# Kernel optimization log

Hardware: AMD Instinct MI355X
Metric: run time of the kernel (lower is better)

## Reference

```python
import jax, jax.numpy as jnp
import numpy as np

HEADS = 4
RATES = (1, 2, 3, 4)
BN_EPS = 1e-5


def setup_inputs() -> dict:
    key = jax.random.key(0)
    k1, k2, k3 = jax.random.split(key, 3)
    b, c, h, w = 4, 256, 128, 128
    x = jax.random.normal(k1, (b, c, h, w), dtype=jnp.float32)
    w_qkv = jax.random.normal(k2, (3 * c, c), dtype=jnp.float32) * 0.02
    w_proj = jax.random.normal(k3, (c, c), dtype=jnp.float32) * 0.02
    gamma = jnp.ones((c,), dtype=jnp.float32)
    beta = jnp.zeros((c,), dtype=jnp.float32)
    return {"x": x, "w_qkv": w_qkv, "w_proj": w_proj, "gamma": gamma, "beta": beta}


def _neighbors(t, r, h, w):
    # t: [b, d, h, w] -> [b, d, 9, h, w], 3x3 dilated window with zero padding
    # (row-major kernel-position order matches F.unfold's C x kh x kw layout).
    tp = jnp.pad(t, ((0, 0), (0, 0), (r, r), (r, r)))
    return jnp.stack(
        [tp[:, :, i * r:i * r + h, j * r:j * r + w] for i in range(3) for j in range(3)],
        axis=2,
    )


def reference(x, w_qkv, w_proj, gamma, beta):
    b, c, h, w = x.shape
    d = c // HEADS
    # 1x1 conv == channel matmul
    qkv = jnp.einsum('oc,bchw->bohw', w_qkv, x)
    q, k, v = jnp.split(qkv, 3, axis=1)
    q = q.reshape(b, HEADS, d, h, w)
    k = k.reshape(b, HEADS, d, h, w)
    v = v.reshape(b, HEADS, d, h, w)
    outs = []
    for hi, r in enumerate(RATES):
        qh = q[:, hi]                      # [b, d, h, w]
        k_n = _neighbors(k[:, hi], r, h, w)  # [b, d, 9, h, w]
        v_n = _neighbors(v[:, hi], r, h, w)  # [b, d, 9, h, w]
        scores = jnp.einsum('bdhw,bdnhw->bnhw', qh, k_n)  # [b, 9, h, w]
        attn = jax.nn.softmax(scores, axis=1)
        outs.append(jnp.einsum('bdnhw,bnhw->bdhw', v_n, attn))
    y = jnp.concatenate(outs, axis=1)      # [b, c, h, w]
    y = jnp.einsum('oc,bchw->bohw', w_proj, y)
    # BatchNorm2d (training-mode batch statistics, biased variance)
    mean = y.mean(axis=(0, 2, 3), keepdims=True)
    var = ((y - mean) ** 2).mean(axis=(0, 2, 3), keepdims=True)
    yn = (y - mean) * jax.lax.rsqrt(var + BN_EPS)
    yn = yn * gamma[None, :, None, None] + beta[None, :, None, None]
    return x + jax.nn.silu(yn)
```

## Files before the change

kernel.cpp:

```cpp
#include <hip/hip_runtime.h>
#include <hip/hip_bf16.h>

#define BATCH 4
#define CCH   256
#define HH    128
#define WW    128
#define HWSZ  (HH * WW)
#define NHEADS 4
#define DHEAD 64
#define KDIM  256
#define PDIM  16384

typedef unsigned short u16;
typedef short bf16x8 __attribute__((ext_vector_type(8)));
typedef float f32x4  __attribute__((ext_vector_type(4)));

__device__ __forceinline__ float bf2f(u16 u) {
    return __uint_as_float(((unsigned)u) << 16);
}
__device__ __forceinline__ u16 f2bf(float f) {
    unsigned u = __float_as_uint(f);
    unsigned r = (u + 0x7fffu + ((u >> 16) & 1u)) >> 16;
    return (u16)r;
}
__device__ __forceinline__ unsigned pack2(float a, float b) {
    return (unsigned)f2bf(a) | ((unsigned)f2bf(b) << 16);
}
__device__ __forceinline__ void gl_lds16(const u16* g, u16* l) {
    __builtin_amdgcn_global_load_lds(
        (const __attribute__((address_space(1))) void*)g,
        (__attribute__((address_space(3))) void*)l, 16, 0, 0);
}

__global__ __launch_bounds__(256) void wconv(
    const float* __restrict__ wq, const float* __restrict__ wp,
    u16* __restrict__ wqb, u16* __restrict__ wpb)
{
    const int i = (blockIdx.x * 256 + threadIdx.x) * 4;
    const float4 v = (i < 196608)
        ? *reinterpret_cast<const float4*>(&wq[i])
        : *reinterpret_cast<const float4*>(&wp[i - 196608]);
    ushort4 o;
    o.x = f2bf(v.x); o.y = f2bf(v.y); o.z = f2bf(v.z); o.w = f2bf(v.w);
    if (i < 196608) *reinterpret_cast<ushort4*>(&wqb[i]) = o;
    else            *reinterpret_cast<ushort4*>(&wpb[i - 196608]) = o;
}

__global__ __launch_bounds__(256) void transpose_x(
    const float* __restrict__ x, u16* __restrict__ XT)
{
    __shared__ float t[32][33];
    const int b  = blockIdx.z;
    const int c0 = blockIdx.y * 32;
    const int p0 = blockIdx.x * 32;
    const int tid = threadIdx.x;

    #pragma unroll
    for (int it = 0; it < 4; ++it) {
        const int r = it * 8 + (tid >> 5);
        const int col = tid & 31;
        t[r][col] = x[((size_t)b * CCH + c0 + r) * HWSZ + p0 + col];
    }
    __syncthreads();
    #pragma unroll
    for (int it = 0; it < 2; ++it) {
        const int prow = it * 16 + (tid >> 4);
        const int cpair = (tid & 15) * 2;
        const float v0 = t[cpair][prow];
        const float v1 = t[cpair + 1][prow];
        ushort2 o; o.x = f2bf(v0); o.y = f2bf(v1);
        *reinterpret_cast<ushort2*>(
            &XT[((size_t)b * HWSZ + p0 + prow) * CCH + c0 + cpair]) = o;
    }
}

__global__ __launch_bounds__(256) void gemm_qkv(
    const u16* __restrict__ A, const u16* __restrict__ B,
    u16* __restrict__ QKVH, long long b_zs)
{
    constexpr int BK = 64;
    constexpr int CTP = 72;
    __shared__ __align__(16) u16 lds[18432];
    u16* As = lds;
    u16* Bs = lds + 8192;

    const int tid  = threadIdx.x;
    const int lane = tid & 63;
    const int w    = tid >> 6;
    const int wm   = w >> 1, wn = w & 1;
    const int o0   = blockIdx.y * 128;
    const int p0   = blockIdx.x * 128;
    const int z    = blockIdx.z;
    const u16* Bz  = B + (size_t)z * b_zs;

    const int srow  = lane >> 3;
    const int sslot = (lane & 7) ^ srow;

    auto stage = [&](int c0) {
        #pragma unroll
        for (int j = 0; j < 4; ++j) {
            const int q = w * 4 + j;
            const int r = q * 8 + srow;
            gl_lds16(A  + (size_t)(o0 + r) * KDIM + c0 + sslot * 8, As + q * 512);
            gl_lds16(Bz + (size_t)(p0 + r) * KDIM + c0 + sslot * 8, Bs + q * 512);
        }
    };

    f32x4 acc[4][4];
    #pragma unroll
    for (int m = 0; m < 4; ++m)
        #pragma unroll
        for (int n = 0; n < 4; ++n)
            acc[m][n] = (f32x4){0.f, 0.f, 0.f, 0.f};

    stage(0);
    #pragma unroll
    for (int kt = 0; kt < KDIM / BK; ++kt) {
        __syncthreads();
        #pragma unroll
        for (int h = 0; h < 2; ++h) {
            bf16x8 af[4], bfr[4];
            #pragma unroll
            for (int m = 0; m < 4; ++m) {
                const int r  = wm * 64 + m * 16 + (lane & 15);
                const int sl = ((h << 2) | (lane >> 4)) ^ (r & 7);
                af[m] = *reinterpret_cast<const bf16x8*>(As + r * BK + sl * 8);
            }
            #pragma unroll
            for (int n = 0; n < 4; ++n) {
                const int r  = wn * 64 + n * 16 + (lane & 15);
                const int sl = ((h << 2) | (lane >> 4)) ^ (r & 7);
                bfr[n] = *reinterpret_cast<const bf16x8*>(Bs + r * BK + sl * 8);
            }
            #pragma unroll
            for (int m = 0; m < 4; ++m)
                #pragma unroll
                for (int n = 0; n < 4; ++n)
                    acc[m][n] = __builtin_amdgcn_mfma_f32_16x16x32_bf16(
                        af[m], bfr[n], acc[m][n], 0, 0, 0);
        }
        if (kt + 1 < KDIM / BK) {
            __syncthreads();
            stage((kt + 1) * BK);
        }
    }

    __syncthreads();
    u16* Ct = lds;
    const int g = lane >> 4, ln15 = lane & 15;
    #pragma unroll
    for (int m = 0; m < 4; ++m) {
        const int och = m * 16 + g * 4;
        #pragma unroll
        for (int n = 0; n < 4; ++n) {
            const int px = wn * 64 + n * 16 + ln15;
            uint2 w2;
            w2.x = pack2(acc[m][n][0], acc[m][n][1]);
            w2.y = pack2(acc[m][n][2], acc[m][n][3]);
            *reinterpret_cast<uint2*>(&Ct[(wm * 128 + px) * CTP + och]) = w2;
        }
    }
    __syncthreads();

    const int c   = tid & 7;
    const int sl  = (tid >> 3) & 1;
    const int px0 = tid >> 4;
    const int abs_slice = blockIdx.y * 2 + sl;
    const int qkv  = abs_slice >> 2;
    const int head = abs_slice & 3;
    u16* dbase = QKVH + ((size_t)(z * NHEADS + head) * HWSZ) * 192 + qkv * 64 + c * 8;
    #pragma unroll
    for (int pass = 0; pass < 8; ++pass) {
        const int px = px0 + pass * 16;
        const uint4 val = *reinterpret_cast<const uint4*>(
            &Ct[(sl * 128 + px) * CTP + c * 8]);
        *reinterpret_cast<uint4*>(dbase + (size_t)(p0 + px) * 192) = val;
    }
}

__global__ __launch_bounds__(256) void attn_proj(
    const u16* __restrict__ QKVH, const u16* __restrict__ WP,
    u16* __restrict__ YP, float* __restrict__ part, int batch0)
{
    __shared__ u16 y_lds[32][264];
    const int tid = threadIdx.x;
    const int z   = blockIdx.z;
    const int batch = batch0 + z;
    const int bxr = blockIdx.x;
    const int bx  = (bxr & 7) * 64 + (bxr >> 3);
    const int pxl = tid >> 3;
    const int oct = tid & 7;
    const int p   = bx * 32 + pxl;
    const int yy = p >> 7, xx = p & 127;

    #pragma unroll 1
    for (int hi = 0; hi < NHEADS; ++hi) {
        const int r = hi + 1;
        const u16* base = QKVH + ((size_t)(z * NHEADS + hi) * HWSZ) * 192;

        const uint4 qv = *reinterpret_cast<const uint4*>(
            base + (size_t)p * 192 + oct * 8);
        float qf[8];
        {
            const unsigned wv[4] = {qv.x, qv.y, qv.z, qv.w};
            #pragma unroll
            for (int d = 0; d < 4; ++d) {
                qf[d * 2 + 0] = __uint_as_float(wv[d] << 16);
                qf[d * 2 + 1] = __uint_as_float(wv[d] & 0xffff0000u);
            }
        }

        int offs[9]; float valid[9];
        #pragma unroll
        for (int n = 0; n < 9; ++n) {
            const int dy = (n / 3 - 1) * r;
            const int dx = (n % 3 - 1) * r;
            const int y2 = yy + dy, x2 = xx + dx;
            const bool ok = (y2 >= 0) && (y2 < HH) && (x2 >= 0) && (x2 < WW);
            valid[n] = ok ? 1.f : 0.f;
            const int y2c = min(max(y2, 0), HH - 1);
            const int x2c = min(max(x2, 0), WW - 1);
            offs[n] = y2c * WW + x2c;
        }

        float sc[9];
        #pragma unroll
        for (int n = 0; n < 9; ++n) {
            const uint4 kv = *reinterpret_cast<const uint4*>(
                base + (size_t)offs[n] * 192 + 64 + oct * 8);
            const unsigned wv[4] = {kv.x, kv.y, kv.z, kv.w};
            float s = 0.f;
            #pragma unroll
            for (int d = 0; d < 4; ++d) {
                s += qf[d * 2 + 0] * __uint_as_float(wv[d] << 16);
                s += qf[d * 2 + 1] * __uint_as_float(wv[d] & 0xffff0000u);
            }
            sc[n] = s;
        }
        #pragma unroll
        for (int n = 0; n < 9; ++n) {
            sc[n] += __shfl_xor(sc[n], 1);
            sc[n] += __shfl_xor(sc[n], 2);
            sc[n] += __shfl_xor(sc[n], 4);
            sc[n] *= valid[n];
        }

        float m = sc[0];
        #pragma unroll
        for (int n = 1; n < 9; ++n) m = fmaxf(m, sc[n]);
        float wgt[9], den = 0.f;
        #pragma unroll
        for (int n = 0; n < 9; ++n) { wgt[n] = __expf(sc[n] - m); den += wgt[n]; }
        const float inv = 1.f / den;
        #pragma unroll
        for (int n = 0; n < 9; ++n) wgt[n] *= inv * valid[n];

        float a[8];
        #pragma unroll
        for (int d = 0; d < 8; ++d) a[d] = 0.f;
        #pragma unroll
        for (int n = 0; n < 9; ++n) {
            const uint4 vv = *reinterpret_cast<const uint4*>(
                base + (size_t)offs[n] * 192 + 128 + oct * 8);
            const unsigned wv[4] = {vv.x, vv.y, vv.z, vv.w};
            const float wn_ = wgt[n];
            #pragma unroll
            for (int d = 0; d < 4; ++d) {
                a[d * 2 + 0] += wn_ * __uint_as_float(wv[d] << 16);
                a[d * 2 + 1] += wn_ * __uint_as_float(wv[d] & 0xffff0000u);
            }
        }
        uint4 st;
        st.x = pack2(a[0], a[1]);
        st.y = pack2(a[2], a[3]);
        st.z = pack2(a[4], a[5]);
        st.w = pack2(a[6], a[7]);
        *reinterpret_cast<uint4*>(&y_lds[pxl][hi * 64 + oct * 8]) = st;
    }
    __syncthreads();

    const int lane = tid & 63;
    const int w    = tid >> 6;
    const int ln15 = lane & 15, grp = lane >> 4;

    f32x4 acc[4][2];
    #pragma unroll
    for (int m = 0; m < 4; ++m)
        #pragma unroll
        for (int n = 0; n < 2; ++n)
            acc[m][n] = (f32x4){0.f, 0.f, 0.f, 0.f};

    #pragma unroll
    for (int ks = 0; ks < 8; ++ks) {
        bf16x8 bfr[2];
        #pragma unroll
        for (int n = 0; n < 2; ++n) {
            const int px = n * 16 + ln15;
            bfr[n] = *reinterpret_cast<const bf16x8*>(
                &y_lds[px][(ks * 4 + grp) * 8]);
        }
        bf16x8 af[4];
        #pragma unroll
        for (int m = 0; m < 4; ++m) {
            const int row = w * 64 + m * 16 + ln15;
            af[m] = *reinterpret_cast<const bf16x8*>(
                WP + (size_t)row * 256 + ks * 32 + grp * 8);
        }
        #pragma unroll
        for (int m = 0; m < 4; ++m)
            #pragma unroll
            for (int n = 0; n < 2; ++n)
                acc[m][n] = __builtin_amdgcn_mfma_f32_16x16x32_bf16(
                    af[m], bfr[n], acc[m][n], 0, 0, 0);
    }

    u16* Yz = YP + (size_t)batch * CCH * HWSZ;
    float sums[4][4], sqs[4][4];
    #pragma unroll
    for (int m = 0; m < 4; ++m) {
        const int row = w * 64 + m * 16 + grp * 4;
        #pragma unroll
        for (int j = 0; j < 4; ++j) {
            const float v0 = acc[m][0][j], v1 = acc[m][1][j];
            sums[m][j] = v0 + v1;
            sqs[m][j]  = v0 * v0 + v1 * v1;
        }
        #pragma unroll
        for (int n = 0; n < 2; ++n) {
            const int pc = bx * 32 + n * 16 + ln15;
            #pragma unroll
            for (int j = 0; j < 4; ++j)
                Yz[(size_t)(row + j) * PDIM + pc] = f2bf(acc[m][n][j]);
        }
    }
    #pragma unroll
    for (int mask = 1; mask <= 8; mask <<= 1)
        #pragma unroll
        for (int m = 0; m < 4; ++m)
            #pragma unroll
            for (int j = 0; j < 4; ++j) {
                sums[m][j] += __shfl_xor(sums[m][j], mask);
                sqs[m][j]  += __shfl_xor(sqs[m][j],  mask);
            }
    if (ln15 == 0) {
        const int blk = batch * 512 + bx;
        #pragma unroll
        for (int m = 0; m < 4; ++m) {
            const int row = w * 64 + m * 16 + grp * 4;
            #pragma unroll
            for (int j = 0; j < 4; ++j) {
                const size_t idx = ((size_t)(row + j) * 2048 + blk) * 2;
                part[idx]     = sums[m][j];
                part[idx + 1] = sqs[m][j];
            }
        }
    }
}

__global__ __launch_bounds__(256) void bn_final(
    const float* __restrict__ part, float* __restrict__ stats)
{
    const int c = blockIdx.x;
    const int tid = threadIdx.x;
    float s = 0.f, q = 0.f;
    #pragma unroll
    for (int it = 0; it < 8; ++it) {
        const int i = tid + it * 256;
        s += part[((size_t)c * 2048 + i) * 2 + 0];
        q += part[((size_t)c * 2048 + i) * 2 + 1];
    }
    __shared__ float sh0[256], sh1[256];
    sh0[tid] = s; sh1[tid] = q;
    __syncthreads();
    for (int st = 128; st > 0; st >>= 1) {
        if (tid < st) { sh0[tid] += sh0[tid + st]; sh1[tid] += sh1[tid + st]; }
        __syncthreads();
    }
    if (tid == 0) {
        const float N = (float)(BATCH * HWSZ);
        const float mean = sh0[0] / N;
        const float var  = sh1[0] / N - mean * mean;
        stats[c]       = mean;
        stats[CCH + c] = rsqrtf(var + 1e-5f);
    }
}

__global__ __launch_bounds__(256) void bn_silu_res(
    const u16* __restrict__ yp, const float* __restrict__ x,
    const float* __restrict__ stats, const float* __restrict__ gamma,
    const float* __restrict__ beta, float* __restrict__ out)
{
    const size_t i = ((size_t)blockIdx.x * 256 + threadIdx.x) * 8;
    const int c = (int)((i >> 14) & 255);
    const float mean = stats[c];
    const float inv  = stats[CCH + c];
    const float g = gamma[c], bt = beta[c];

    const uint4 yv = *reinterpret_cast<const uint4*>(&yp[i]);
    const unsigned wv[4] = {yv.x, yv.y, yv.z, yv.w};
    float vo[8];
    #pragma unroll
    for (int d = 0; d < 4; ++d) {
        const float y0 = __uint_as_float(wv[d] << 16);
        const float y1 = __uint_as_float(wv[d] & 0xffff0000u);
        const float yn0 = (y0 - mean) * inv * g + bt;
        const float yn1 = (y1 - mean) * inv * g + bt;
        vo[d * 2 + 0] = yn0 / (1.f + __expf(-yn0));
        vo[d * 2 + 1] = yn1 / (1.f + __expf(-yn1));
    }
    const float4 x0 = *reinterpret_cast<const float4*>(&x[i]);
    const float4 x1 = *reinterpret_cast<const float4*>(&x[i + 4]);
    float4 o0, o1;
    o0.x = x0.x + vo[0]; o0.y = x0.y + vo[1];
    o0.z = x0.z + vo[2]; o0.w = x0.w + vo[3];
    o1.x = x1.x + vo[4]; o1.y = x1.y + vo[5];
    o1.z = x1.z + vo[6]; o1.w = x1.w + vo[7];
    *reinterpret_cast<float4*>(&out[i])     = o0;
    *reinterpret_cast<float4*>(&out[i + 4]) = o1;
}

extern "C" void kernel_launch(void* const* d_in, const int* in_sizes, int n_in,
                              void* d_out, int out_size, void* d_ws, size_t ws_size,
                              hipStream_t stream)
{
    const float* x      = (const float*)d_in[0];
    const float* w_qkv  = (const float*)d_in[1];
    const float* w_proj = (const float*)d_in[2];
    const float* gamma  = (const float*)d_in[3];
    const float* beta   = (const float*)d_in[4];
    float* out = (float*)d_out;

    u16*   XT    = (u16*)d_ws;
    u16*   YP    = XT;
    u16*   WQb   = XT + (size_t)BATCH * HWSZ * CCH;
    u16*   WPb   = WQb + 768 * CCH;
    float* part  = (float*)(WPb + CCH * CCH);
    float* stats = part + (size_t)CCH * 2048 * 2;
    u16*   QKVH2 = (u16*)(stats + 512);

    wconv<<<256, 256, 0, stream>>>(w_qkv, w_proj, WQb, WPb);

    transpose_x<<<dim3(HWSZ / 32, CCH / 32, BATCH), 256, 0, stream>>>(x, XT);

    for (int pair = 0; pair < 2; ++pair) {
        const u16* Bx = XT + (size_t)pair * 2 * HWSZ * CCH;
        gemm_qkv<<<dim3(PDIM / 128, 768 / 128, 2), 256, 0, stream>>>(
            WQb, Bx, QKVH2, (long long)HWSZ * CCH);

        attn_proj<<<dim3(HWSZ / 32, 1, 2), 256, 0, stream>>>(
            QKVH2, WPb, YP, part, pair * 2);
    }

    bn_final<<<CCH, 256, 0, stream>>>(part, stats);

    bn_silu_res<<<(unsigned)((size_t)BATCH * CCH * HWSZ / 8 / 256), 256, 0, stream>>>(
        YP, x, stats, gamma, beta, out);
}
```

Before: 163.3 us.

## Assign one head per wave and two lanes per pixel in attention stage

The neighborhood-attention stage of attn_proj no longer loops serially over the four heads with eight lanes per pixel. Each wave now handles one head, and each pixel's 64-dim head is split across two lanes of 32 channels. This removes the head loop and two of the three shuffle-reduction steps, and gives each thread larger contiguous loads. In exchange it raises register use (32-float q and accumulator arrays) and changes the memory access pattern, which could lower occupancy.

```diff
diff --git a/kernel.cpp b/kernel.cpp
--- a/kernel.cpp
+++ b/kernel.cpp
@@ -188,25 +188,29 @@
     const int batch = batch0 + z;
     const int bxr = blockIdx.x;
     const int bx  = (bxr & 7) * 64 + (bxr >> 3);
-    const int pxl = tid >> 3;
-    const int oct = tid & 7;
-    const int p   = bx * 32 + pxl;
-    const int yy = p >> 7, xx = p & 127;
-
-    #pragma unroll 1
-    for (int hi = 0; hi < NHEADS; ++hi) {
-        const int r = hi + 1;
+    const int lane = tid & 63;
+    const int w    = tid >> 6;
+
+    {
+        const int hi   = w;
+        const int pxl  = lane >> 1;
+        const int half = lane & 1;
+        const int p    = bx * 32 + pxl;
+        const int yy = p >> 7, xx = p & 127;
+        const int r  = hi + 1;
         const u16* base = QKVH + ((size_t)(z * NHEADS + hi) * HWSZ) * 192;
 
-        const uint4 qv = *reinterpret_cast<const uint4*>(
-            base + (size_t)p * 192 + oct * 8);
-        float qf[8];
-        {
-            const unsigned wv[4] = {qv.x, qv.y, qv.z, qv.w};
+        const uint4* qp = reinterpret_cast<const uint4*>(
+            base + (size_t)p * 192 + half * 32);
+        float qf[32];
+        #pragma unroll
+        for (int c4 = 0; c4 < 4; ++c4) {
+            const uint4 t = qp[c4];
+            const unsigned wv[4] = {t.x, t.y, t.z, t.w};
             #pragma unroll
             for (int d = 0; d < 4; ++d) {
-                qf[d * 2 + 0] = __uint_as_float(wv[d] << 16);
-                qf[d * 2 + 1] = __uint_as_float(wv[d] & 0xffff0000u);
+                qf[c4 * 8 + d * 2 + 0] = __uint_as_float(wv[d] << 16);
+                qf[c4 * 8 + d * 2 + 1] = __uint_as_float(wv[d] & 0xffff0000u);
             }
         }
 
@@ -226,22 +230,24 @@
         float sc[9];
         #pragma unroll
         for (int n = 0; n < 9; ++n) {
-            const uint4 kv = *reinterpret_cast<const uint4*>(
-                base + (size_t)offs[n] * 192 + 64 + oct * 8);
-            const unsigned wv[4] = {kv.x, kv.y, kv.z, kv.w};
+            const uint4* kp = reinterpret_cast<const uint4*>(
+                base + (size_t)offs[n] * 192 + 64 + half * 32);
             float s = 0.f;
             #pragma unroll
-            for (int d = 0; d < 4; ++d) {
-                s += qf[d * 2 + 0] * __uint_as_float(wv[d] << 16);
-                s += qf[d * 2 + 1] * __uint_as_float(wv[d] & 0xffff0000u);
+            for (int c4 = 0; c4 < 4; ++c4) {
+                const uint4 t = kp[c4];
+                const unsigned wv[4] = {t.x, t.y, t.z, t.w};
+                #pragma unroll
+                for (int d = 0; d < 4; ++d) {
+                    s += qf[c4 * 8 + d * 2 + 0] * __uint_as_float(wv[d] << 16);
+                    s += qf[c4 * 8 + d * 2 + 1] * __uint_as_float(wv[d] & 0xffff0000u);
+                }
             }
             sc[n] = s;
         }
         #pragma unroll
         for (int n = 0; n < 9; ++n) {
             sc[n] += __shfl_xor(sc[n], 1);
-            sc[n] += __shfl_xor(sc[n], 2);
-            sc[n] += __shfl_xor(sc[n], 4);
             sc[n] *= valid[n];
         }
 
@@ -255,32 +261,38 @@
         #pragma unroll
         for (int n = 0; n < 9; ++n) wgt[n] *= inv * valid[n];
 
-        float a[8];
-        #pragma unroll
-        for (int d = 0; d < 8; ++d) a[d] = 0.f;
+        float a[32];
+        #pragma unroll
+        for (int d = 0; d < 32; ++d) a[d] = 0.f;
         #pragma unroll
         for (int n = 0; n < 9; ++n) {
-            const uint4 vv = *reinterpret_cast<const uint4*>(
-                base + (size_t)offs[n] * 192 + 128 + oct * 8);
-            const unsigned wv[4] = {vv.x, vv.y, vv.z, vv.w};
+            const uint4* vp = reinterpret_cast<const uint4*>(
+                base + (size_t)offs[n] * 192 + 128 + half * 32);
             const float wn_ = wgt[n];
             #pragma unroll
-            for (int d = 0; d < 4; ++d) {
-                a[d * 2 + 0] += wn_ * __uint_as_float(wv[d] << 16);
-                a[d * 2 + 1] += wn_ * __uint_as_float(wv[d] & 0xffff0000u);
-            }
-        }
-        uint4 st;
-        st.x = pack2(a[0], a[1]);
-        st.y = pack2(a[2], a[3]);
-        st.z = pack2(a[4], a[5]);
-        st.w = pack2(a[6], a[7]);
-        *reinterpret_cast<uint4*>(&y_lds[pxl][hi * 64 + oct * 8]) = st;
+            for (int c4 = 0; c4 < 4; ++c4) {
+                const uint4 t = vp[c4];
+                const unsigned wv[4] = {t.x, t.y, t.z, t.w};
+                #pragma unroll
+                for (int d = 0; d < 4; ++d) {
+                    a[c4 * 8 + d * 2 + 0] += wn_ * __uint_as_float(wv[d] << 16);
+                    a[c4 * 8 + d * 2 + 1] += wn_ * __uint_as_float(wv[d] & 0xffff0000u);
+                }
+            }
+        }
+        #pragma unroll
+        for (int c4 = 0; c4 < 4; ++c4) {
+            uint4 st;
+            st.x = pack2(a[c4 * 8 + 0], a[c4 * 8 + 1]);
+            st.y = pack2(a[c4 * 8 + 2], a[c4 * 8 + 3]);
+            st.z = pack2(a[c4 * 8 + 4], a[c4 * 8 + 5]);
+            st.w = pack2(a[c4 * 8 + 6], a[c4 * 8 + 7]);
+            *reinterpret_cast<uint4*>(
+                &y_lds[pxl][hi * 64 + half * 32 + c4 * 8]) = st;
+        }
     }
     __syncthreads();
 
-    const int lane = tid & 63;
-    const int w    = tid >> 6;
     const int ln15 = lane & 15, grp = lane >> 4;
 
     f32x4 acc[4][2];
```

New measurement: 175.1 us. 7.2% more time.
